# Kernel tuning notes

Measured on AMD Instinct MI355X. Metric: run time of the kernel, lower is better.

The kernel has to match this reference:

```python
import jax, jax.numpy as jnp
import numpy as np

N_NODES = 20000
N_EDGES = 320000
IN_F = 16
OUT_F = 16
EDGE_DIM = 16
EDGE_HID = 64
BN_EPS = 1e-5


def setup_inputs() -> dict:
    key = jax.random.key(0)
    ks = jax.random.split(key, 12)
    inp = {
        "h_neigh": jax.random.normal(ks[0], (N_NODES, IN_F), dtype=jnp.float32),
        "h_self": jax.random.normal(ks[1], (N_NODES, IN_F), dtype=jnp.float32),
        "edge_features": jax.random.normal(ks[2], (N_EDGES, EDGE_DIM), dtype=jnp.float32),
        "src": jax.random.randint(ks[3], (N_EDGES,), 0, N_NODES),
        "dst": jax.random.randint(ks[4], (N_EDGES,), 0, N_NODES),
        # params (xavier-ish scale)
        "W_self": jax.random.normal(ks[5], (IN_F, OUT_F), dtype=jnp.float32) * (2.0 / (IN_F + OUT_F)) ** 0.5,
        "bn_gamma": jnp.ones((OUT_F,), dtype=jnp.float32),
        "bn_beta": jnp.zeros((OUT_F,), dtype=jnp.float32),
        "We1": jax.random.normal(ks[6], (EDGE_DIM, EDGE_HID), dtype=jnp.float32) * (2.0 / (EDGE_DIM + EDGE_HID)) ** 0.5,
        "be1": jnp.zeros((EDGE_HID,), dtype=jnp.float32),
        "We2": jax.random.normal(ks[7], (EDGE_HID, IN_F * OUT_F), dtype=jnp.float32) * (2.0 / (EDGE_HID + IN_F * OUT_F)) ** 0.5,
        "be2": jnp.zeros((IN_F * OUT_F,), dtype=jnp.float32),
    }
    return inp


def reference(h_neigh, h_self, edge_features, src, dst,
              W_self, bn_gamma, bn_beta, We1, be1, We2, be2):
    n_nodes = h_self.shape[0]
    in_f, out_f = W_self.shape
    # edge MLP -> per-edge weight matrix [E, in_f, out_f]
    eh = jax.nn.relu(edge_features @ We1 + be1)
    edge_w = (eh @ We2 + be2).reshape(-1, in_f, out_f)
    # gather src features, per-edge matvec, scatter-sum to dst
    # (sum over in_f commutes with the edge sum-reduce, matching
    #  update_all(u_mul_e, sum) followed by .sum(dim=1))
    msg = jnp.einsum('ei,eio->eo', h_neigh[src], edge_w)  # [E, out_f]
    neigh = jax.ops.segment_sum(msg, dst, num_segments=n_nodes)  # [N, out_f]
    # fc_self: Linear(no bias) -> BatchNorm1d (training stats) -> tanh
    y = h_self @ W_self
    mu = y.mean(axis=0)
    var = y.var(axis=0)
    y = (y - mu) / jnp.sqrt(var + BN_EPS) * bn_gamma + bn_beta
    y = jnp.tanh(y)
    z = jax.nn.relu(y + neigh)
    z_norm = jnp.linalg.norm(z, axis=1, keepdims=True)
    z_norm = jnp.where(z_norm == 0, jnp.ones_like(z_norm), z_norm)
    return z / z_norm
```

## Files before the change

kernel.cpp:

```cpp
#include <hip/hip_runtime.h>
#include <hip/hip_bf16.h>
#include <math.h>

#define NN 20000
#define NE 320000
#define BN_EPS 1e-5f
#define CAP 64

#define MSG_BYTES   (NE * 16 * 4)
#define ELIST_OFF   MSG_BYTES
#define ELIST_BYTES (NN * CAP * 4)
#define CNT_OFF     (ELIST_OFF + ELIST_BYTES)
#define CNT_BYTES   (NN * 4)
#define BNACC_OFF   (CNT_OFF + CNT_BYTES)
#define EXTRA_OFF   (BNACC_OFF + 128)
#define EXTRA_BYTES (NN * 16 * 4)
#define Y_OFF       (EXTRA_OFF + EXTRA_BYTES)
#define ZERO_OFF    CNT_OFF
#define ZERO_BYTES  (CNT_BYTES + 128 + EXTRA_BYTES)

typedef __bf16 bf16x8 __attribute__((ext_vector_type(8)));
typedef float  f32x4  __attribute__((ext_vector_type(4)));

union BF8 { bf16x8 v; unsigned short us[8]; unsigned int ui[4]; };

__device__ __forceinline__ unsigned short f2bf(float f) {
    unsigned int u = __builtin_bit_cast(unsigned int, f);
    u += 0x7FFFu + ((u >> 16) & 1u);
    return (unsigned short)(u >> 16);
}
__device__ __forceinline__ float bf2f(unsigned short s) {
    unsigned int u = ((unsigned int)s) << 16;
    return __builtin_bit_cast(float, u);
}
__device__ __forceinline__ unsigned int pack2bf(float a, float b) {
    return (unsigned int)f2bf(a) | ((unsigned int)f2bf(b) << 16);
}

__global__ __launch_bounds__(256, 4) void edge_kernel(
    const float* __restrict__ h_neigh, const float* __restrict__ efeat,
    const int* __restrict__ src, const int* __restrict__ dst,
    const float* __restrict__ We1, const float* __restrict__ be1,
    const float* __restrict__ We2, const float* __restrict__ be2,
    float* __restrict__ msgb, int* __restrict__ elist,
    int* __restrict__ cnt, float* __restrict__ extra,
    const float* __restrict__ h_self, const float* __restrict__ Wsf,
    float* __restrict__ y, float* __restrict__ bnacc)
{
    __shared__ __align__(16) unsigned short A3sw[16 * 2 * 64 * 8];
    __shared__ float red[4][32];

    const int t = threadIdx.x;

    {
        const float4* W2v = (const float4*)We2;
#pragma unroll
        for (int it = 0; it < 16; it++) {
            int c4 = t + 256 * it;
            float4 w = W2v[c4];
            int f = c4 * 4;
            int h = f >> 8, c = f & 255;
            int mb = c >> 4, kb = h >> 5, hh = h & 31, co = c & 15;
            int base = ((mb * 2 + kb) * 64 + (hh >> 3) * 16) * 8 + (hh & 7);
            A3sw[base + (co + 0) * 8] = f2bf(w.x);
            A3sw[base + (co + 1) * 8] = f2bf(w.y);
            A3sw[base + (co + 2) * 8] = f2bf(w.z);
            A3sw[base + (co + 3) * 8] = f2bf(w.w);
        }
    }
    __syncthreads();

    const int L = t & 63, wv = t >> 6;
    const int lo16 = L & 15, q = L >> 4;
    const int qc = q & 1;
    const bool qlow = (q < 2);
    const bool qhi1 = ((q >> 1) != 0);

    BF8 w1h[4], w1l[4];
#pragma unroll
    for (int c = 0; c < 4; c++) {
#pragma unroll
        for (int j = 0; j < 8; j++) {
            float w;
            if (q < 2)                 w = We1[(q * 8 + j) * 64 + c * 16 + lo16];
            else if (q == 2 && j == 0) w = be1[c * 16 + lo16];
            else                       w = 0.f;
            unsigned short h = f2bf(w);
            w1h[c].us[j] = h;
            w1l[c].us[j] = f2bf(w - bf2f(h));
        }
    }

    BF8 be2T;
#pragma unroll
    for (int j = 0; j < 8; j++) {
        float bv = be2[(qc * 8 + j) * 16 + lo16];
        be2T.us[j] = qlow ? f2bf(bv) : (unsigned short)0;
    }

    const int addrA = (((q & 1) * 2 + 0) * 16 + lo16) * 4;
    const int addrB = (((q & 1) * 2 + 1) * 16 + lo16) * 4;

    for (int bt = blockIdx.x; bt < NE / 64; bt += gridDim.x) {
        int e = bt * 64 + wv * 16 + lo16;
        int se = src[e];
        int de = dst[e];

        int kv = 0;
        if (q == 0) {
            kv = atomicAdd(&cnt[de], 1);
            if (kv < CAP) elist[de * CAP + kv] = e;
        }

        float xr[16];
        {
            const float4* xp = (const float4*)(h_neigh + (size_t)se * 16);
#pragma unroll
            for (int k4 = 0; k4 < 4; k4++) {
                float4 a = xp[k4];
                xr[k4*4+0] = a.x; xr[k4*4+1] = a.y; xr[k4*4+2] = a.z; xr[k4*4+3] = a.w;
            }
        }

        BF8 a2h, a2l;
        {
            const float4* ep = (const float4*)(efeat + (size_t)e * 16 + qc * 8);
            float4 e0 = ep[0], e1 = ep[1];
            float ev[8] = {e0.x, e0.y, e0.z, e0.w, e1.x, e1.y, e1.z, e1.w};
#pragma unroll
            for (int j = 0; j < 8; j++) {
                if (qlow) {
                    unsigned short h = f2bf(ev[j]);
                    a2h.us[j] = h;
                    a2l.us[j] = f2bf(ev[j] - bf2f(h));
                } else {
                    a2h.us[j] = (q == 2 && j == 0) ? (unsigned short)0x3F80 : (unsigned short)0;
                    a2l.us[j] = 0;
                }
            }
        }

        float vch[4][4];
#pragma unroll
        for (int c = 0; c < 4; c++) {
            f32x4 c2 = {0.f, 0.f, 0.f, 0.f};
            c2 = __builtin_amdgcn_mfma_f32_16x16x32_bf16(w1h[c].v, a2h.v, c2, 0, 0, 0);
            c2 = __builtin_amdgcn_mfma_f32_16x16x32_bf16(w1l[c].v, a2h.v, c2, 0, 0, 0);
            c2 = __builtin_amdgcn_mfma_f32_16x16x32_bf16(w1h[c].v, a2l.v, c2, 0, 0, 0);
#pragma unroll
            for (int r = 0; r < 4; r++) vch[c][r] = fmaxf(c2[r], 0.f);
        }

        unsigned int dwH[4][2], dwL[4][2];
#pragma unroll
        for (int c = 0; c < 4; c++) {
#pragma unroll
            for (int d = 0; d < 2; d++) {
                float va = vch[c][2*d], vb = vch[c][2*d+1];
                unsigned short ha = f2bf(va), hb = f2bf(vb);
                dwH[c][d] = (unsigned int)ha | ((unsigned int)hb << 16);
                dwL[c][d] = pack2bf(va - bf2f(ha), vb - bf2f(hb));
            }
        }

        BF8 b3h[2], b3l[2];
#pragma unroll
        for (int kb = 0; kb < 2; kb++) {
#pragma unroll
            for (int tt = 0; tt < 4; tt++) {
                int d = tt & 1;
                int addr = (tt >> 1) ? addrB : addrA;
                int h0 = __builtin_amdgcn_ds_bpermute(addr, (int)dwH[kb*2+0][d]);
                int h1 = __builtin_amdgcn_ds_bpermute(addr, (int)dwH[kb*2+1][d]);
                int l0 = __builtin_amdgcn_ds_bpermute(addr, (int)dwL[kb*2+0][d]);
                int l1 = __builtin_amdgcn_ds_bpermute(addr, (int)dwL[kb*2+1][d]);
                b3h[kb].ui[tt] = (unsigned int)(qhi1 ? h1 : h0);
                b3l[kb].ui[tt] = (unsigned int)(qhi1 ? l1 : l0);
            }
        }

        BF8 xT;
#pragma unroll
        for (int j = 0; j < 8; j++)
            xT.us[j] = qlow ? f2bf(xr[qc * 8 + j]) : (unsigned short)0;
        f32x4 msg = {0.f, 0.f, 0.f, 0.f};
        msg = __builtin_amdgcn_mfma_f32_16x16x32_bf16(be2T.v, xT.v, msg, 0, 0, 0);

#pragma unroll 4
        for (int mb = 0; mb < 16; mb++) {
            bf16x8 a3a = *(const bf16x8*)&A3sw[((mb * 2 + 0) * 64 + L) * 8];
            bf16x8 a3b = *(const bf16x8*)&A3sw[((mb * 2 + 1) * 64 + L) * 8];
            f32x4 acc = {0.f, 0.f, 0.f, 0.f};
            acc = __builtin_amdgcn_mfma_f32_16x16x32_bf16(a3a, b3h[0].v, acc, 0, 0, 0);
            acc = __builtin_amdgcn_mfma_f32_16x16x32_bf16(a3b, b3h[1].v, acc, 0, 0, 0);
            acc = __builtin_amdgcn_mfma_f32_16x16x32_bf16(a3a, b3l[0].v, acc, 0, 0, 0);
            acc = __builtin_amdgcn_mfma_f32_16x16x32_bf16(a3b, b3l[1].v, acc, 0, 0, 0);
            float xm = xr[mb];
            msg[0] += xm * acc[0];
            msg[1] += xm * acc[1];
            msg[2] += xm * acc[2];
            msg[3] += xm * acc[3];
        }

        int kk = __shfl(kv, lo16);
        if (kk < CAP) {
            *(float4*)(msgb + (size_t)e * 16 + q * 4) =
                make_float4(msg[0], msg[1], msg[2], msg[3]);
        } else {
            float* xp = extra + (size_t)de * 16 + q * 4;
#pragma unroll
            for (int r = 0; r < 4; r++) atomicAdd(xp + r, msg[r]);
        }
    }

    int sb = (int)blockIdx.x - 945;
    if (sb >= 0 && sb < 79) {
        int n = sb * 256 + t;
        bool act = (n < NN);
        float hv[16], yv[16];
        if (act) {
            const float4* h4 = (const float4*)(h_self + (size_t)n * 16);
#pragma unroll
            for (int k = 0; k < 4; k++) {
                float4 a = h4[k];
                hv[4*k+0] = a.x; hv[4*k+1] = a.y; hv[4*k+2] = a.z; hv[4*k+3] = a.w;
            }
        } else {
#pragma unroll
            for (int i = 0; i < 16; i++) hv[i] = 0.f;
        }
#pragma unroll
        for (int o = 0; o < 16; o++) {
            float a = 0.f;
#pragma unroll
            for (int i = 0; i < 16; i++) a += hv[i] * Wsf[i*16 + o];
            yv[o] = a;
        }
        if (act) {
            float4* y4 = (float4*)(y + (size_t)n * 16);
#pragma unroll
            for (int k = 0; k < 4; k++)
                y4[k] = make_float4(yv[4*k+0], yv[4*k+1], yv[4*k+2], yv[4*k+3]);
        }
        int lane = t & 63;
#pragma unroll
        for (int o = 0; o < 16; o++) {
            float a = act ? yv[o] : 0.f;
            float b = act ? yv[o]*yv[o] : 0.f;
#pragma unroll
            for (int off = 32; off > 0; off >>= 1) {
                a += __shfl_down(a, off);
                b += __shfl_down(b, off);
            }
            if (lane == 0) { red[wv][o] = a; red[wv][16 + o] = b; }
        }
        __syncthreads();
        if (t < 32) {
            float s = red[0][t] + red[1][t] + red[2][t] + red[3][t];
            atomicAdd(&bnacc[t], s);
        }
    }
}

__global__ __launch_bounds__(256) void final_kernel(
    const float* __restrict__ msgb, const int* __restrict__ elist,
    const int* __restrict__ cnt, const float* __restrict__ extra,
    const float* __restrict__ y, const float* __restrict__ bnacc,
    const float* __restrict__ gamma, const float* __restrict__ beta,
    float* __restrict__ out)
{
    int tb = blockIdx.x * 256 + threadIdx.x;
    int n = tb >> 2, c = tb & 3;
    if (n >= NN) return;

    int deg = cnt[n];
    int m = deg < CAP ? deg : CAP;
    const float4* m4 = (const float4*)msgb;
    const int* el = elist + n * CAP;

    float ax = 0.f, ay = 0.f, az = 0.f, aw = 0.f;
    int k = 0;
    for (; k + 4 <= m; k += 4) {
        int e0 = el[k], e1 = el[k+1], e2 = el[k+2], e3 = el[k+3];
        float4 a0 = m4[(size_t)e0*4 + c];
        float4 a1 = m4[(size_t)e1*4 + c];
        float4 a2 = m4[(size_t)e2*4 + c];
        float4 a3 = m4[(size_t)e3*4 + c];
        ax += (a0.x + a1.x) + (a2.x + a3.x);
        ay += (a0.y + a1.y) + (a2.y + a3.y);
        az += (a0.z + a1.z) + (a2.z + a3.z);
        aw += (a0.w + a1.w) + (a2.w + a3.w);
    }
    for (; k < m; k++) {
        int e0 = el[k];
        float4 a0 = m4[(size_t)e0*4 + c];
        ax += a0.x; ay += a0.y; az += a0.z; aw += a0.w;
    }
    if (deg > CAP) {
        float4 a0 = *(const float4*)(extra + (size_t)n * 16 + c * 4);
        ax += a0.x; ay += a0.y; az += a0.z; aw += a0.w;
    }

    float4 yv4 = ((const float4*)y)[(size_t)n * 4 + c];
    float yv[4] = {yv4.x, yv4.y, yv4.z, yv4.w};
    float nb[4] = {ax, ay, az, aw};

    const float inv_n = 1.f / (float)NN;
    float z[4];
    float ss = 0.f;
#pragma unroll
    for (int r = 0; r < 4; r++) {
        int o = c * 4 + r;
        float mu  = bnacc[o] * inv_n;
        float var = bnacc[16 + o] * inv_n - mu * mu;
        float inv = rsqrtf(var + BN_EPS);
        float yy  = (yv[r] - mu) * inv * gamma[o] + beta[o];
        float tt  = tanhf(yy);
        float zz  = fmaxf(tt + nb[r], 0.f);
        z[r] = zz;
        ss += zz * zz;
    }
    ss += __shfl_xor(ss, 1);
    ss += __shfl_xor(ss, 2);
    float nrm = sqrtf(ss);
    if (nrm == 0.f) nrm = 1.f;
    float rr = 1.f / nrm;
    *(float4*)(out + (size_t)n * 16 + c * 4) =
        make_float4(z[0]*rr, z[1]*rr, z[2]*rr, z[3]*rr);
}

extern "C" void kernel_launch(void* const* d_in, const int* in_sizes, int n_in,
                              void* d_out, int out_size, void* d_ws, size_t ws_size,
                              hipStream_t stream) {
    const float* h_neigh = (const float*)d_in[0];
    const float* h_self  = (const float*)d_in[1];
    const float* efeat   = (const float*)d_in[2];
    const int*   src     = (const int*)d_in[3];
    const int*   dst     = (const int*)d_in[4];
    const float* W_self  = (const float*)d_in[5];
    const float* gamma   = (const float*)d_in[6];
    const float* beta    = (const float*)d_in[7];
    const float* We1     = (const float*)d_in[8];
    const float* be1     = (const float*)d_in[9];
    const float* We2     = (const float*)d_in[10];
    const float* be2     = (const float*)d_in[11];
    float* out = (float*)d_out;

    char* ws = (char*)d_ws;
    float* msgb  = (float*)ws;
    int*   elist = (int*)(ws + ELIST_OFF);
    int*   cnt   = (int*)(ws + CNT_OFF);
    float* bnacc = (float*)(ws + BNACC_OFF);
    float* extra = (float*)(ws + EXTRA_OFF);
    float* y     = (float*)(ws + Y_OFF);

    hipMemsetAsync(ws + ZERO_OFF, 0, ZERO_BYTES, stream);

    edge_kernel<<<1024, 256, 0, stream>>>(
        h_neigh, efeat, src, dst, We1, be1, We2, be2,
        msgb, elist, cnt, extra,
        h_self, W_self, y, bnacc);
    final_kernel<<<(NN * 4 + 255) / 256, 256, 0, stream>>>(
        msgb, elist, cnt, extra, y, bnacc, gamma, beta, out);
}
```

Before: 155.9 us.

## Software-pipeline edge index loads and degree atomics, pad per-node counters

The edge loop is restructured so the next tile's src/dst loads and degree-counter atomicAdd are issued before the current tile's MFMA work, hiding atomic and index latency. Per-node counters are padded to a 64-byte stride to cut atomic contention from false sharing. The edge-list write is moved after the message store, and the edge-list cap is lowered from 64 to 48, shrinking that buffer. This costs a larger counter array to zero in the memset and more edges spilling onto the slow atomic overflow path for high-degree nodes.

```diff
diff --git a/kernel.cpp b/kernel.cpp
--- a/kernel.cpp
+++ b/kernel.cpp
@@ -5,13 +5,14 @@
 #define NN 20000
 #define NE 320000
 #define BN_EPS 1e-5f
-#define CAP 64
+#define CAP 48
+#define CNTP 16
 
 #define MSG_BYTES   (NE * 16 * 4)
 #define ELIST_OFF   MSG_BYTES
 #define ELIST_BYTES (NN * CAP * 4)
 #define CNT_OFF     (ELIST_OFF + ELIST_BYTES)
-#define CNT_BYTES   (NN * 4)
+#define CNT_BYTES   (NN * CNTP * 4)
 #define BNACC_OFF   (CNT_OFF + CNT_BYTES)
 #define EXTRA_OFF   (BNACC_OFF + 128)
 #define EXTRA_BYTES (NN * 16 * 4)
@@ -43,7 +44,7 @@
     const float* __restrict__ We1, const float* __restrict__ be1,
     const float* __restrict__ We2, const float* __restrict__ be2,
     float* __restrict__ msgb, int* __restrict__ elist,
-    int* __restrict__ cnt, float* __restrict__ extra,
+    int* __restrict__ cntp, float* __restrict__ extra,
     const float* __restrict__ h_self, const float* __restrict__ Wsf,
     float* __restrict__ y, float* __restrict__ bnacc)
 {
@@ -101,115 +102,130 @@
     const int addrA = (((q & 1) * 2 + 0) * 16 + lo16) * 4;
     const int addrB = (((q & 1) * 2 + 1) * 16 + lo16) * 4;
 
-    for (int bt = blockIdx.x; bt < NE / 64; bt += gridDim.x) {
+    const int NT = NE / 64;
+    int bt = blockIdx.x;
+    {
         int e = bt * 64 + wv * 16 + lo16;
         int se = src[e];
         int de = dst[e];
-
         int kv = 0;
-        if (q == 0) {
-            kv = atomicAdd(&cnt[de], 1);
-            if (kv < CAP) elist[de * CAP + kv] = e;
-        }
-
-        float xr[16];
-        {
-            const float4* xp = (const float4*)(h_neigh + (size_t)se * 16);
-#pragma unroll
-            for (int k4 = 0; k4 < 4; k4++) {
-                float4 a = xp[k4];
-                xr[k4*4+0] = a.x; xr[k4*4+1] = a.y; xr[k4*4+2] = a.z; xr[k4*4+3] = a.w;
-            }
-        }
-
-        BF8 a2h, a2l;
-        {
-            const float4* ep = (const float4*)(efeat + (size_t)e * 16 + qc * 8);
-            float4 e0 = ep[0], e1 = ep[1];
-            float ev[8] = {e0.x, e0.y, e0.z, e0.w, e1.x, e1.y, e1.z, e1.w};
-#pragma unroll
-            for (int j = 0; j < 8; j++) {
-                if (qlow) {
-                    unsigned short h = f2bf(ev[j]);
-                    a2h.us[j] = h;
-                    a2l.us[j] = f2bf(ev[j] - bf2f(h));
-                } else {
-                    a2h.us[j] = (q == 2 && j == 0) ? (unsigned short)0x3F80 : (unsigned short)0;
-                    a2l.us[j] = 0;
+        if (q == 0) kv = atomicAdd(&cntp[de * CNTP], 1);
+
+        while (true) {
+            int btn = bt + gridDim.x;
+            bool hn = btn < NT;
+            int en = 0, sen = 0, den = 0, kvn = 0;
+            if (hn) {
+                en = btn * 64 + wv * 16 + lo16;
+                sen = src[en];
+                den = dst[en];
+                if (q == 0) kvn = atomicAdd(&cntp[den * CNTP], 1);
+            }
+
+            float xr[16];
+            {
+                const float4* xp = (const float4*)(h_neigh + (size_t)se * 16);
+#pragma unroll
+                for (int k4 = 0; k4 < 4; k4++) {
+                    float4 a = xp[k4];
+                    xr[k4*4+0] = a.x; xr[k4*4+1] = a.y; xr[k4*4+2] = a.z; xr[k4*4+3] = a.w;
                 }
             }
-        }
-
-        float vch[4][4];
-#pragma unroll
-        for (int c = 0; c < 4; c++) {
-            f32x4 c2 = {0.f, 0.f, 0.f, 0.f};
-            c2 = __builtin_amdgcn_mfma_f32_16x16x32_bf16(w1h[c].v, a2h.v, c2, 0, 0, 0);
-            c2 = __builtin_amdgcn_mfma_f32_16x16x32_bf16(w1l[c].v, a2h.v, c2, 0, 0, 0);
-            c2 = __builtin_amdgcn_mfma_f32_16x16x32_bf16(w1h[c].v, a2l.v, c2, 0, 0, 0);
-#pragma unroll
-            for (int r = 0; r < 4; r++) vch[c][r] = fmaxf(c2[r], 0.f);
-        }
-
-        unsigned int dwH[4][2], dwL[4][2];
-#pragma unroll
-        for (int c = 0; c < 4; c++) {
-#pragma unroll
-            for (int d = 0; d < 2; d++) {
-                float va = vch[c][2*d], vb = vch[c][2*d+1];
-                unsigned short ha = f2bf(va), hb = f2bf(vb);
-                dwH[c][d] = (unsigned int)ha | ((unsigned int)hb << 16);
-                dwL[c][d] = pack2bf(va - bf2f(ha), vb - bf2f(hb));
-            }
-        }
-
-        BF8 b3h[2], b3l[2];
-#pragma unroll
-        for (int kb = 0; kb < 2; kb++) {
-#pragma unroll
-            for (int tt = 0; tt < 4; tt++) {
-                int d = tt & 1;
-                int addr = (tt >> 1) ? addrB : addrA;
-                int h0 = __builtin_amdgcn_ds_bpermute(addr, (int)dwH[kb*2+0][d]);
-                int h1 = __builtin_amdgcn_ds_bpermute(addr, (int)dwH[kb*2+1][d]);
-                int l0 = __builtin_amdgcn_ds_bpermute(addr, (int)dwL[kb*2+0][d]);
-                int l1 = __builtin_amdgcn_ds_bpermute(addr, (int)dwL[kb*2+1][d]);
-                b3h[kb].ui[tt] = (unsigned int)(qhi1 ? h1 : h0);
-                b3l[kb].ui[tt] = (unsigned int)(qhi1 ? l1 : l0);
-            }
-        }
-
-        BF8 xT;
-#pragma unroll
-        for (int j = 0; j < 8; j++)
-            xT.us[j] = qlow ? f2bf(xr[qc * 8 + j]) : (unsigned short)0;
-        f32x4 msg = {0.f, 0.f, 0.f, 0.f};
-        msg = __builtin_amdgcn_mfma_f32_16x16x32_bf16(be2T.v, xT.v, msg, 0, 0, 0);
+
+            BF8 a2h, a2l;
+            {
+                const float4* ep = (const float4*)(efeat + (size_t)e * 16 + qc * 8);
+                float4 e0 = ep[0], e1 = ep[1];
+                float ev[8] = {e0.x, e0.y, e0.z, e0.w, e1.x, e1.y, e1.z, e1.w};
+#pragma unroll
+                for (int j = 0; j < 8; j++) {
+                    if (qlow) {
+                        unsigned short h = f2bf(ev[j]);
+                        a2h.us[j] = h;
+                        a2l.us[j] = f2bf(ev[j] - bf2f(h));
+                    } else {
+                        a2h.us[j] = (q == 2 && j == 0) ? (unsigned short)0x3F80 : (unsigned short)0;
+                        a2l.us[j] = 0;
+                    }
+                }
+            }
+
+            float vch[4][4];
+#pragma unroll
+            for (int c = 0; c < 4; c++) {
+                f32x4 c2 = {0.f, 0.f, 0.f, 0.f};
+                c2 = __builtin_amdgcn_mfma_f32_16x16x32_bf16(w1h[c].v, a2h.v, c2, 0, 0, 0);
+                c2 = __builtin_amdgcn_mfma_f32_16x16x32_bf16(w1l[c].v, a2h.v, c2, 0, 0, 0);
+                c2 = __builtin_amdgcn_mfma_f32_16x16x32_bf16(w1h[c].v, a2l.v, c2, 0, 0, 0);
+#pragma unroll
+                for (int r = 0; r < 4; r++) vch[c][r] = fmaxf(c2[r], 0.f);
+            }
+
+            unsigned int dwH[4][2], dwL[4][2];
+#pragma unroll
+            for (int c = 0; c < 4; c++) {
+#pragma unroll
+                for (int d = 0; d < 2; d++) {
+                    float va = vch[c][2*d], vb = vch[c][2*d+1];
+                    unsigned short ha = f2bf(va), hb = f2bf(vb);
+                    dwH[c][d] = (unsigned int)ha | ((unsigned int)hb << 16);
+                    dwL[c][d] = pack2bf(va - bf2f(ha), vb - bf2f(hb));
+                }
+            }
+
+            BF8 b3h[2], b3l[2];
+#pragma unroll
+            for (int kb = 0; kb < 2; kb++) {
+#pragma unroll
+                for (int tt = 0; tt < 4; tt++) {
+                    int d = tt & 1;
+                    int addr = (tt >> 1) ? addrB : addrA;
+                    int h0 = __builtin_amdgcn_ds_bpermute(addr, (int)dwH[kb*2+0][d]);
+                    int h1 = __builtin_amdgcn_ds_bpermute(addr, (int)dwH[kb*2+1][d]);
+                    int l0 = __builtin_amdgcn_ds_bpermute(addr, (int)dwL[kb*2+0][d]);
+                    int l1 = __builtin_amdgcn_ds_bpermute(addr, (int)dwL[kb*2+1][d]);
+                    b3h[kb].ui[tt] = (unsigned int)(qhi1 ? h1 : h0);
+                    b3l[kb].ui[tt] = (unsigned int)(qhi1 ? l1 : l0);
+                }
+            }
+
+            BF8 xT;
+#pragma unroll
+            for (int j = 0; j < 8; j++)
+                xT.us[j] = qlow ? f2bf(xr[qc * 8 + j]) : (unsigned short)0;
+            f32x4 msg = {0.f, 0.f, 0.f, 0.f};
+            msg = __builtin_amdgcn_mfma_f32_16x16x32_bf16(be2T.v, xT.v, msg, 0, 0, 0);
 
 #pragma unroll 4
-        for (int mb = 0; mb < 16; mb++) {
-            bf16x8 a3a = *(const bf16x8*)&A3sw[((mb * 2 + 0) * 64 + L) * 8];
-            bf16x8 a3b = *(const bf16x8*)&A3sw[((mb * 2 + 1) * 64 + L) * 8];
-            f32x4 acc = {0.f, 0.f, 0.f, 0.f};
-            acc = __builtin_amdgcn_mfma_f32_16x16x32_bf16(a3a, b3h[0].v, acc, 0, 0, 0);
-            acc = __builtin_amdgcn_mfma_f32_16x16x32_bf16(a3b, b3h[1].v, acc, 0, 0, 0);
-            acc = __builtin_amdgcn_mfma_f32_16x16x32_bf16(a3a, b3l[0].v, acc, 0, 0, 0);
-            acc = __builtin_amdgcn_mfma_f32_16x16x32_bf16(a3b, b3l[1].v, acc, 0, 0, 0);
-            float xm = xr[mb];
-            msg[0] += xm * acc[0];
-            msg[1] += xm * acc[1];
-            msg[2] += xm * acc[2];
-            msg[3] += xm * acc[3];
-        }
-
-        int kk = __shfl(kv, lo16);
-        if (kk < CAP) {
+            for (int mb = 0; mb < 16; mb++) {
+                bf16x8 a3a = *(const bf16x8*)&A3sw[((mb * 2 + 0) * 64 + L) * 8];
+                bf16x8 a3b = *(const bf16x8*)&A3sw[((mb * 2 + 1) * 64 + L) * 8];
+                f32x4 acc = {0.f, 0.f, 0.f, 0.f};
+                acc = __builtin_amdgcn_mfma_f32_16x16x32_bf16(a3a, b3h[0].v, acc, 0, 0, 0);
+                acc = __builtin_amdgcn_mfma_f32_16x16x32_bf16(a3b, b3h[1].v, acc, 0, 0, 0);
+                acc = __builtin_amdgcn_mfma_f32_16x16x32_bf16(a3a, b3l[0].v, acc, 0, 0, 0);
+                acc = __builtin_amdgcn_mfma_f32_16x16x32_bf16(a3b, b3l[1].v, acc, 0, 0, 0);
+                float xm = xr[mb];
+                msg[0] += xm * acc[0];
+                msg[1] += xm * acc[1];
+                msg[2] += xm * acc[2];
+                msg[3] += xm * acc[3];
+            }
+
             *(float4*)(msgb + (size_t)e * 16 + q * 4) =
                 make_float4(msg[0], msg[1], msg[2], msg[3]);
-        } else {
-            float* xp = extra + (size_t)de * 16 + q * 4;
-#pragma unroll
-            for (int r = 0; r < 4; r++) atomicAdd(xp + r, msg[r]);
+
+            int kk = __shfl(kv, lo16);
+            if (kk < CAP) {
+                if (q == 0) elist[de * CAP + kv] = e;
+            } else {
+                float* xp = extra + (size_t)de * 16 + q * 4;
+#pragma unroll
+                for (int r = 0; r < 4; r++) atomicAdd(xp + r, msg[r]);
+            }
+
+            if (!hn) break;
+            bt = btn; e = en; se = sen; de = den; kv = kvn;
         }
     }
 
@@ -264,7 +280,7 @@
 
 __global__ __launch_bounds__(256) void final_kernel(
     const float* __restrict__ msgb, const int* __restrict__ elist,
-    const int* __restrict__ cnt, const float* __restrict__ extra,
+    const int* __restrict__ cntp, const float* __restrict__ extra,
     const float* __restrict__ y, const float* __restrict__ bnacc,
     const float* __restrict__ gamma, const float* __restrict__ beta,
     float* __restrict__ out)
@@ -273,7 +289,7 @@
     int n = tb >> 2, c = tb & 3;
     if (n >= NN) return;
 
-    int deg = cnt[n];
+    int deg = cntp[n * CNTP];
     int m = deg < CAP ? deg : CAP;
     const float4* m4 = (const float4*)msgb;
     const int* el = elist + n * CAP;
@@ -349,7 +365,7 @@
     char* ws = (char*)d_ws;
     float* msgb  = (float*)ws;
     int*   elist = (int*)(ws + ELIST_OFF);
-    int*   cnt   = (int*)(ws + CNT_OFF);
+    int*   cntp  = (int*)(ws + CNT_OFF);
     float* bnacc = (float*)(ws + BNACC_OFF);
     float* extra = (float*)(ws + EXTRA_OFF);
     float* y     = (float*)(ws + Y_OFF);
@@ -358,8 +374,8 @@
 
     edge_kernel<<<1024, 256, 0, stream>>>(
         h_neigh, efeat, src, dst, We1, be1, We2, be2,
-        msgb, elist, cnt, extra,
+        msgb, elist, cntp, extra,
         h_self, W_self, y, bnacc);
     final_kernel<<<(NN * 4 + 255) / 256, 256, 0, stream>>>(
-        msgb, elist, cnt, extra, y, bnacc, gamma, beta, out);
-}
+        msgb, elist, cntp, extra, y, bnacc, gamma, beta, out);
+}
```

Result: no change. 155.6 us (-0.2%).
